# Performance work log

Measured on AMD Instinct MI355X. Metric: run time of the kernel, lower is better.

## Reference

```python
import jax, jax.numpy as jnp
import numpy as np

H = W = 56; WS = 7; SHIFT = 3; NH = 6; DIM = 192; DEPTH = 2
HD = DIM // NH; NW = (H // WS) * (W // WS); N = WS * WS; SCALE = HD ** -0.5

# relative position index (constant, as in WindowAttention.__init__)
_c = np.stack(np.meshgrid(np.arange(WS), np.arange(WS), indexing='ij')).reshape(2, -1)
_r = (_c[:, :, None] - _c[:, None, :]).transpose(1, 2, 0)
_r[..., 0] += WS - 1; _r[..., 1] += WS - 1; _r[..., 0] *= 2 * WS - 1
RPI = jnp.asarray(_r.sum(-1).reshape(-1))  # (N*N,)

def _build_mask():
    # shifted-window attention mask (constant, built in SwinTransformerBlock.__init__)
    img = np.zeros((H, W))
    sl = (slice(0, -WS), slice(-WS, -SHIFT), slice(-SHIFT, None))
    cnt = 0
    for hs in sl:
        for ws_ in sl:
            img[hs, ws_] = cnt; cnt += 1
    mw = img.reshape(H // WS, WS, W // WS, WS).transpose(0, 2, 1, 3).reshape(-1, N)
    am = mw[:, None, :] - mw[:, :, None]  # (nW, N, N)
    return jnp.asarray(np.where(am != 0, -100.0, 0.0).astype(np.float32))

MASK = _build_mask()

def _ln(x, g, b):
    m = jnp.mean(x, -1, keepdims=True)
    v = jnp.mean((x - m) ** 2, -1, keepdims=True)
    return (x - m) * jax.lax.rsqrt(v + 1e-5) * g + b

def setup_inputs() -> dict:
    key = jax.random.key(0)
    ks = jax.random.split(key, 8)
    B = 64; s = 0.02
    return {
        'x': jax.random.normal(ks[0], (B, H * W, DIM), jnp.float32),
        'norm1_g': jnp.ones((DEPTH, DIM), jnp.float32),
        'norm1_b': jnp.zeros((DEPTH, DIM), jnp.float32),
        'qkv_w': jax.random.normal(ks[1], (DEPTH, DIM, 3 * DIM), jnp.float32) * s,
        'qkv_b': jnp.zeros((DEPTH, 3 * DIM), jnp.float32),
        'rpb': jax.random.normal(ks[2], (DEPTH, (2 * WS - 1) ** 2, NH), jnp.float32) * s,
        'proj_w': jax.random.normal(ks[3], (DEPTH, DIM, DIM), jnp.float32) * s,
        'proj_b': jnp.zeros((DEPTH, DIM), jnp.float32),
        'norm2_g': jnp.ones((DEPTH, DIM), jnp.float32),
        'norm2_b': jnp.zeros((DEPTH, DIM), jnp.float32),
        'fc1_w': jax.random.normal(ks[4], (DEPTH, DIM, 4 * DIM), jnp.float32) * s,
        'fc1_b': jnp.zeros((DEPTH, 4 * DIM), jnp.float32),
        'fc2_w': jax.random.normal(ks[5], (DEPTH, 4 * DIM, DIM), jnp.float32) * s,
        'fc2_b': jnp.zeros((DEPTH, DIM), jnp.float32),
    }

def reference(x, norm1_g, norm1_b, qkv_w, qkv_b, rpb, proj_w, proj_b,
              norm2_g, norm2_b, fc1_w, fc1_b, fc2_w, fc2_b):
    B = x.shape[0]
    for i in range(DEPTH):
        shift = 0 if i % 2 == 0 else WS // 2
        # --- windowed MHSA branch ---
        h = _ln(x, norm1_g[i], norm1_b[i]).reshape(B, H, W, DIM)
        if shift:
            h = jnp.roll(h, (-shift, -shift), (1, 2))
        # window partition -> (B*nW, N, C)
        w = h.reshape(B, H // WS, WS, W // WS, WS, DIM)
        w = w.transpose(0, 1, 3, 2, 4, 5).reshape(B * NW, N, DIM)
        qkv = (w @ qkv_w[i] + qkv_b[i]).reshape(B * NW, N, 3, NH, HD)
        qkv = qkv.transpose(2, 0, 3, 1, 4)  # (3, Bw, NH, N, HD)
        q, k, v = qkv[0] * SCALE, qkv[1], qkv[2]
        attn = jnp.einsum('bhnd,bhmd->bhnm', q, k)  # (Bw, NH, N, N)
        bias = rpb[i][RPI].reshape(N, N, NH).transpose(2, 0, 1)
        attn = attn + bias[None]
        if shift:
            attn = attn.reshape(B, NW, NH, N, N) + MASK[None, :, None]
            attn = attn.reshape(B * NW, NH, N, N)
        attn = jax.nn.softmax(attn, axis=-1)
        o = jnp.einsum('bhnm,bhmd->bhnd', attn, v)
        o = o.transpose(0, 2, 1, 3).reshape(B * NW, N, DIM)
        o = o @ proj_w[i] + proj_b[i]
        # window reverse
        h = o.reshape(B, H // WS, W // WS, WS, WS, DIM)
        h = h.transpose(0, 1, 3, 2, 4, 5).reshape(B, H, W, DIM)
        if shift:
            h = jnp.roll(h, (shift, shift), (1, 2))
        x = x + h.reshape(B, H * W, DIM)
        # --- MLP branch ---
        m = _ln(x, norm2_g[i], norm2_b[i])
        m = jax.nn.gelu(m @ fc1_w[i] + fc1_b[i], approximate=False)
        x = x + (m @ fc2_w[i] + fc2_b[i])
    return x
```

## Files before the change

### kernel.cpp

```cpp
#include <hip/hip_runtime.h>
#include <stdint.h>

#define NTOK   49
#define BATCH  64
#define MROWS  (BATCH * 64 * NTOK)
#define SCALE_ 0.17677669529663687f

typedef __attribute__((ext_vector_type(8))) short bf16x8;
typedef __attribute__((ext_vector_type(4))) float f32x4;

union V8 { uint4 u; unsigned short s[8]; };

__device__ __forceinline__ float bf2f(unsigned short u) {
  union { unsigned int i; float f; } c; c.i = ((unsigned int)u) << 16; return c.f;
}
__device__ __forceinline__ unsigned short f2bf(float f) {
  union { float f; unsigned int i; } c; c.f = f;
  unsigned int lsb = (c.i >> 16) & 1;
  return (unsigned short)((c.i + 0x7fffu + lsb) >> 16);
}

__global__ __launch_bounds__(256) void wt_k(const float* __restrict__ W,
    unsigned short* __restrict__ Wt, int K, int N)
{
  int idx = blockIdx.x * 256 + threadIdx.x;
  if (idx < K * N) {
    int k = idx / N, n = idx - k * N;
    Wt[(size_t)n * K + k] = f2bf(W[idx]);
  }
}

__global__ __launch_bounds__(256) void ln_k(const float* __restrict__ X,
    const float* __restrict__ g, const float* __restrict__ b,
    unsigned short* __restrict__ out, int shift)
{
  int wr = blockIdx.x * 4 + (threadIdx.x >> 6);
  int lane = threadIdx.x & 63;
  int win = wr / 49, n = wr % 49;
  int bi = win >> 6, w64 = win & 63;
  int wh = w64 >> 3, ww = w64 & 7;
  int ti = n / 7, tj = n % 7;
  int gh = wh * 7 + ti + shift; if (gh >= 56) gh -= 56;
  int gw = ww * 7 + tj + shift; if (gw >= 56) gw -= 56;
  size_t srow = (size_t)bi * 3136 + gh * 56 + gw;
  const float* xr = X + srow * 192;
  float v0 = xr[lane], v1 = xr[lane + 64], v2 = xr[lane + 128];
  float s  = v0 + v1 + v2;
  float s2 = v0*v0 + v1*v1 + v2*v2;
  #pragma unroll
  for (int m = 32; m >= 1; m >>= 1) { s += __shfl_xor(s, m); s2 += __shfl_xor(s2, m); }
  float mean = s * (1.0f/192.0f);
  float var  = s2 * (1.0f/192.0f) - mean*mean;
  float inv  = rsqrtf(var + 1e-5f);
  unsigned short* orow = out + (size_t)wr * 192;
  orow[lane]       = f2bf((v0-mean)*inv*g[lane]      + b[lane]);
  orow[lane+64]    = f2bf((v1-mean)*inv*g[lane+64]   + b[lane+64]);
  orow[lane+128]   = f2bf((v2-mean)*inv*g[lane+128]  + b[lane+128]);
}

template<int EPI>
__global__ __launch_bounds__(256, 4) void gemm2_k(
    const unsigned short* __restrict__ A,
    const unsigned short* __restrict__ Wt,
    const float* __restrict__ bias,
    unsigned short* __restrict__ Cbf,
    const float* __restrict__ Xres,
    float* __restrict__ Xdst,
    int N, int shift)
{
  __shared__ unsigned short As[128][40];
  const int tid = threadIdx.x;
  const int lane = tid & 63, wv = tid >> 6;
  const int wm = wv >> 1, wn = wv & 1;
  const int row0 = blockIdx.x * 128;
  const int n0   = blockIdx.y * 64;
  const int fr = lane & 15, kq = (lane >> 4) * 8;
  bf16x8 bfr[6][2];
  #pragma unroll
  for (int ks = 0; ks < 6; ++ks)
    #pragma unroll
    for (int ni = 0; ni < 2; ++ni)
      bfr[ks][ni] = *reinterpret_cast<const bf16x8*>(
          &Wt[(size_t)(n0 + wn*32 + ni*16 + fr) * 192 + ks*32 + kq]);
  const int sr  = tid >> 1, ssg = (tid & 1) * 16;
  const unsigned short* arow = A + (size_t)(row0 + sr) * 192 + ssg;
  uint4 a0 = *reinterpret_cast<const uint4*>(arow);
  uint4 a1 = *reinterpret_cast<const uint4*>(arow + 8);
  f32x4 acc[4][2] = {};
  #pragma unroll
  for (int ks = 0; ks < 6; ++ks) {
    __syncthreads();
    *reinterpret_cast<uint4*>(&As[sr][ssg])     = a0;
    *reinterpret_cast<uint4*>(&As[sr][ssg + 8]) = a1;
    if (ks < 5) {
      a0 = *reinterpret_cast<const uint4*>(arow + (ks+1)*32);
      a1 = *reinterpret_cast<const uint4*>(arow + (ks+1)*32 + 8);
    }
    __syncthreads();
    #pragma unroll
    for (int mi = 0; mi < 4; ++mi) {
      bf16x8 afr = *reinterpret_cast<const bf16x8*>(&As[wm*64 + mi*16 + fr][kq]);
      #pragma unroll
      for (int ni = 0; ni < 2; ++ni)
        acc[mi][ni] = __builtin_amdgcn_mfma_f32_16x16x32_bf16(afr, bfr[ks][ni], acc[mi][ni], 0, 0, 0);
    }
  }
  const int lcol = lane & 15, lr4 = (lane >> 4) * 4;
  #pragma unroll
  for (int mi = 0; mi < 4; ++mi)
  #pragma unroll
  for (int ni = 0; ni < 2; ++ni)
  #pragma unroll
  for (int i = 0; i < 4; ++i) {
    int gr = row0 + wm*64 + mi*16 + lr4 + i;
    int gc = n0 + wn*32 + ni*16 + lcol;
    float v = acc[mi][ni][i] + bias[gc];
    if (EPI == 0) {
      Cbf[(size_t)gr * N + gc] = f2bf(v);
    } else {
      int win = gr / 49, n = gr % 49;
      int bi = win >> 6, w64 = win & 63;
      int wh = w64 >> 3, ww = w64 & 7;
      int ti = n / 7, tj = n % 7;
      int gh = wh*7 + ti + shift; if (gh >= 56) gh -= 56;
      int gw = ww*7 + tj + shift; if (gw >= 56) gw -= 56;
      size_t idx = ((size_t)bi * 3136 + gh * 56 + gw) * 192 + gc;
      Xdst[idx] = Xres[idx] + v;
    }
  }
}

__global__ __launch_bounds__(256, 3) void mlp_k(
    const float* __restrict__ X,
    const float* __restrict__ g, const float* __restrict__ b,
    const unsigned short* __restrict__ W1t,
    const float* __restrict__ b1,
    const unsigned short* __restrict__ W2t,
    const float* __restrict__ b2,
    float* __restrict__ Y)
{
  __shared__ unsigned short As[32][200];
  __shared__ unsigned short Hs[32][200];
  const int row0 = blockIdx.x * 32;
  const int tid = threadIdx.x, lane = tid & 63, wv = tid >> 6;
  #pragma unroll
  for (int r = 0; r < 8; ++r) {
    int row = wv * 8 + r;
    const float* xr = X + (size_t)(row0 + row) * 192;
    float v0 = xr[lane], v1 = xr[lane + 64], v2 = xr[lane + 128];
    float s  = v0 + v1 + v2;
    float s2 = v0*v0 + v1*v1 + v2*v2;
    #pragma unroll
    for (int m = 32; m >= 1; m >>= 1) { s += __shfl_xor(s, m); s2 += __shfl_xor(s2, m); }
    float mean = s * (1.0f/192.0f);
    float var  = s2 * (1.0f/192.0f) - mean*mean;
    float inv  = rsqrtf(var + 1e-5f);
    As[row][lane]       = f2bf((v0-mean)*inv*g[lane]      + b[lane]);
    As[row][lane+64]    = f2bf((v1-mean)*inv*g[lane+64]   + b[lane+64]);
    As[row][lane+128]   = f2bf((v2-mean)*inv*g[lane+128]  + b[lane+128]);
  }
  __syncthreads();
  const int fr = lane & 15, kq = (lane >> 4) * 8;
  const int lcol = lane & 15, lr4 = (lane >> 4) * 4;
  f32x4 acc2[2][3] = {};
  #pragma unroll
  for (int q = 0; q < 4; ++q) {
    bf16x8 bw1[6][3];
    #pragma unroll
    for (int ks = 0; ks < 6; ++ks)
      #pragma unroll
      for (int ni = 0; ni < 3; ++ni)
        bw1[ks][ni] = *reinterpret_cast<const bf16x8*>(
            &W1t[(size_t)(q*192 + wv*48 + ni*16 + fr) * 192 + ks*32 + kq]);
    f32x4 acc1[2][3] = {};
    #pragma unroll
    for (int ks = 0; ks < 6; ++ks) {
      #pragma unroll
      for (int mi = 0; mi < 2; ++mi) {
        bf16x8 afr = *reinterpret_cast<const bf16x8*>(&As[mi*16 + fr][ks*32 + kq]);
        #pragma unroll
        for (int ni = 0; ni < 3; ++ni)
          acc1[mi][ni] = __builtin_amdgcn_mfma_f32_16x16x32_bf16(afr, bw1[ks][ni], acc1[mi][ni], 0, 0, 0);
      }
    }
    bf16x8 bw2[6][3];
    #pragma unroll
    for (int ks = 0; ks < 6; ++ks)
      #pragma unroll
      for (int ni = 0; ni < 3; ++ni)
        bw2[ks][ni] = *reinterpret_cast<const bf16x8*>(
            &W2t[(size_t)(wv*48 + ni*16 + fr) * 768 + q*192 + ks*32 + kq]);
    __syncthreads();
    #pragma unroll
    for (int mi = 0; mi < 2; ++mi)
    #pragma unroll
    for (int ni = 0; ni < 3; ++ni)
    #pragma unroll
    for (int i = 0; i < 4; ++i) {
      int rr = mi*16 + lr4 + i;
      int cc = wv*48 + ni*16 + lcol;
      float v = acc1[mi][ni][i] + b1[q*192 + cc];
      float gv = 0.5f * v * (1.0f + erff(v * 0.70710678118654752f));
      Hs[rr][cc] = f2bf(gv);
    }
    __syncthreads();
    #pragma unroll
    for (int ks = 0; ks < 6; ++ks) {
      #pragma unroll
      for (int mi = 0; mi < 2; ++mi) {
        bf16x8 afr = *reinterpret_cast<const bf16x8*>(&Hs[mi*16 + fr][ks*32 + kq]);
        #pragma unroll
        for (int ni = 0; ni < 3; ++ni)
          acc2[mi][ni] = __builtin_amdgcn_mfma_f32_16x16x32_bf16(afr, bw2[ks][ni], acc2[mi][ni], 0, 0, 0);
      }
    }
  }
  #pragma unroll
  for (int mi = 0; mi < 2; ++mi)
  #pragma unroll
  for (int ni = 0; ni < 3; ++ni)
  #pragma unroll
  for (int i = 0; i < 4; ++i) {
    int grow = row0 + mi*16 + lr4 + i;
    int gc = wv*48 + ni*16 + lcol;
    float v = acc2[mi][ni][i] + b2[gc];
    size_t idx = (size_t)grow * 192 + gc;
    Y[idx] = X[idx] + v;
  }
}

template<bool SHIFTED>
__global__ __launch_bounds__(64) void attn_k(
    const unsigned short* __restrict__ qkv,
    const float* __restrict__ rpb,
    unsigned short* __restrict__ out)
{
  __shared__ float kv[2][49][32];
  int blk = blockIdx.x;
  int win = blk / 6, h = blk - win * 6;
  int lane = threadIdx.x;
  const unsigned short* base = qkv + (size_t)win * 49 * 576;
  for (int idx = lane; idx < 196; idx += 64) {
    int n = idx >> 2, sg = (idx & 3) * 8;
    V8 kk, vv;
    kk.u = *reinterpret_cast<const uint4*>(base + n*576 + 192 + h*32 + sg);
    vv.u = *reinterpret_cast<const uint4*>(base + n*576 + 384 + h*32 + sg);
    #pragma unroll
    for (int j = 0; j < 8; ++j) { kv[0][n][sg+j] = bf2f(kk.s[j]); kv[1][n][sg+j] = bf2f(vv.s[j]); }
  }
  __syncthreads();
  if (lane < 49) {
    float q[32];
    const unsigned short* qr = base + (size_t)lane * 576 + h * 32;
    #pragma unroll
    for (int sg = 0; sg < 4; ++sg) {
      V8 qq; qq.u = *reinterpret_cast<const uint4*>(qr + sg*8);
      #pragma unroll
      for (int j = 0; j < 8; ++j) q[sg*8+j] = bf2f(qq.s[j]) * SCALE_;
    }
    int ti = lane / 7, tj = lane - ti * 7;
    int wi = win & 63, wh = wi >> 3, ww = wi & 7;
    int rid = 0;
    if (SHIFTED) {
      int hh = wh*7 + ti, wg = ww*7 + tj;
      rid = (hh < 49 ? 0 : (hh < 53 ? 1 : 2)) * 3 + (wg < 49 ? 0 : (wg < 53 ? 1 : 2));
    }
    float s[49];
    float mx = -1e30f;
    #pragma unroll
    for (int m = 0; m < 49; ++m) {
      float a = 0.f;
      #pragma unroll
      for (int d4 = 0; d4 < 8; ++d4) {
        float4 kf = *reinterpret_cast<const float4*>(&kv[0][m][d4*4]);
        a += q[d4*4+0]*kf.x + q[d4*4+1]*kf.y + q[d4*4+2]*kf.z + q[d4*4+3]*kf.w;
      }
      int mi = m / 7, mj = m - mi * 7;
      a += rpb[((ti - mi + 6) * 13 + (tj - mj + 6)) * 6 + h];
      if (SHIFTED) {
        int hh = wh*7 + mi, wg = ww*7 + mj;
        int rid2 = (hh < 49 ? 0 : (hh < 53 ? 1 : 2)) * 3 + (wg < 49 ? 0 : (wg < 53 ? 1 : 2));
        if (rid2 != rid) a -= 100.f;
      }
      s[m] = a;
      mx = fmaxf(mx, a);
    }
    float sum = 0.f;
    #pragma unroll
    for (int m = 0; m < 49; ++m) { float e = __expf(s[m] - mx); s[m] = e; sum += e; }
    float rs = 1.f / sum;
    float o[32];
    #pragma unroll
    for (int d = 0; d < 32; ++d) o[d] = 0.f;
    #pragma unroll
    for (int m = 0; m < 49; ++m) {
      float p = s[m] * rs;
      #pragma unroll
      for (int d4 = 0; d4 < 8; ++d4) {
        float4 vf = *reinterpret_cast<const float4*>(&kv[1][m][d4*4]);
        o[d4*4+0] += p*vf.x; o[d4*4+1] += p*vf.y; o[d4*4+2] += p*vf.z; o[d4*4+3] += p*vf.w;
      }
    }
    unsigned short* orow = out + ((size_t)win * 49 + lane) * 192 + h * 32;
    #pragma unroll
    for (int sg = 0; sg < 4; ++sg) {
      V8 pk;
      #pragma unroll
      for (int j = 0; j < 8; ++j) pk.s[j] = f2bf(o[sg*8+j]);
      *reinterpret_cast<uint4*>(orow + sg*8) = pk.u;
    }
  }
}

extern "C" void kernel_launch(void* const* d_in, const int* in_sizes, int n_in,
                              void* d_out, int out_size, void* d_ws, size_t ws_size,
                              hipStream_t stream) {
  const float* x    = (const float*)d_in[0];
  const float* n1g  = (const float*)d_in[1];
  const float* n1b  = (const float*)d_in[2];
  const float* qkvw = (const float*)d_in[3];
  const float* qkvb = (const float*)d_in[4];
  const float* rpb  = (const float*)d_in[5];
  const float* pw   = (const float*)d_in[6];
  const float* pb   = (const float*)d_in[7];
  const float* n2g  = (const float*)d_in[8];
  const float* n2b  = (const float*)d_in[9];
  const float* f1w  = (const float*)d_in[10];
  const float* f1b  = (const float*)d_in[11];
  const float* f2w  = (const float*)d_in[12];
  const float* f2b  = (const float*)d_in[13];
  float* out = (float*)d_out;

  const size_t XBYTES = (size_t)MROWS * 192 * 4;
  const size_t ABYTES = (size_t)MROWS * 192 * 2;
  const size_t QBYTES = (size_t)MROWS * 576 * 2;
  char* ws = (char*)d_ws;
  float* x1 = (float*)ws;
  unsigned short* Abuf = (unsigned short*)(ws + XBYTES);
  unsigned short* Bbuf = (unsigned short*)(ws + XBYTES + ABYTES);
  unsigned short* WT   = (unsigned short*)(ws + XBYTES + ABYTES + QBYTES);
  const size_t WQ = 110592, WP = 36864, W1 = 147456, W2 = 147456;
  const size_t WD = WQ + WP + W1 + W2;

  for (int d = 0; d < 2; ++d) {
    unsigned short* wt = WT + d * WD;
    wt_k<<<(int)((WQ + 255)/256), 256, 0, stream>>>(qkvw + (size_t)d*WQ, wt,                 192, 576);
    wt_k<<<(int)((WP + 255)/256), 256, 0, stream>>>(pw   + (size_t)d*WP, wt + WQ,            192, 192);
    wt_k<<<(int)((W1 + 255)/256), 256, 0, stream>>>(f1w  + (size_t)d*W1, wt + WQ + WP,       192, 768);
    wt_k<<<(int)((W2 + 255)/256), 256, 0, stream>>>(f2w  + (size_t)d*W2, wt + WQ + WP + W1,  768, 192);
  }

  const int LNBLK = MROWS / 4;
  const dim3 G_QKV(MROWS/128, 9), G_P(MROWS/128, 3);

  for (int i = 0; i < 2; ++i) {
    int shift = i ? 3 : 0;
    const float* xin = i ? (const float*)x1 : x;
    float* xfin = i ? out : x1;
    const unsigned short* wt = WT + i * WD;
    ln_k<<<LNBLK, 256, 0, stream>>>(xin, n1g + i*192, n1b + i*192, Abuf, shift);
    gemm2_k<0><<<G_QKV, 256, 0, stream>>>(Abuf, wt, qkvb + i*576, Bbuf, nullptr, nullptr, 576, 0);
    if (shift) attn_k<true ><<<BATCH*64*6, 64, 0, stream>>>(Bbuf, rpb + i*169*6, Abuf);
    else       attn_k<false><<<BATCH*64*6, 64, 0, stream>>>(Bbuf, rpb + i*169*6, Abuf);
    gemm2_k<1><<<G_P, 256, 0, stream>>>(Abuf, wt + WQ, pb + i*192, nullptr, xin, x1, 192, shift);
    mlp_k<<<MROWS/32, 256, 0, stream>>>(x1, n2g + i*192, n2b + i*192,
                                        wt + WQ + WP, f1b + i*768,
                                        wt + WQ + WP + W1, f2b + i*192, xfin);
  }
}
```

Baseline: 1.968 ms.

## Fuse LN into QKV GEMM, split MLP into fc1/fc2 with full-K LDS tiles

Layernorm is folded into the QKV and fc1 GEMM kernels, which now hold the whole 128x192 A tile in XOR-swizzled LDS and loop over all output panels in one block. The fused MLP kernel is split into fc1 (writing the GELU hidden tensor to global memory, reusing the QKV buffer) and fc2 (streaming that hidden tensor through LDS with direct global-to-LDS loads). The goal is to drop the separate LN pass and make the MLP's small 32-row tiles more MFMA-efficient. In exchange the hidden activations now make an extra round trip through HBM, and each block keeps a large LDS footprint.

```diff
diff --git a/kernel.cpp b/kernel.cpp
--- a/kernel.cpp
+++ b/kernel.cpp
@@ -1,14 +1,11 @@
 #include <hip/hip_runtime.h>
 #include <stdint.h>
 
-#define NTOK   49
-#define BATCH  64
-#define MROWS  (BATCH * 64 * NTOK)
+#define MROWS  200704
 #define SCALE_ 0.17677669529663687f
 
 typedef __attribute__((ext_vector_type(8))) short bf16x8;
 typedef __attribute__((ext_vector_type(4))) float f32x4;
-
 union V8 { uint4 u; unsigned short s[8]; };
 
 __device__ __forceinline__ float bf2f(unsigned short u) {
@@ -20,6 +17,61 @@
   return (unsigned short)((c.i + 0x7fffu + lsb) >> 16);
 }
 
+typedef __attribute__((address_space(1))) const void gas_t;
+typedef __attribute__((address_space(3))) void las_t;
+__device__ __forceinline__ void gload16(const void* g, void* l) {
+  __builtin_amdgcn_global_load_lds((gas_t*)g, (las_t*)l, 16, 0, 0);
+}
+
+__device__ __forceinline__ bf16x8 ard(const unsigned short* As, int row, int k) {
+  return *reinterpret_cast<const bf16x8*>(As + row * 192 + (((k >> 3) ^ (row & 7)) << 3));
+}
+__device__ __forceinline__ void awr(unsigned short* As, int row, int c, unsigned short v) {
+  As[row * 192 + (((c >> 3) ^ (row & 7)) << 3) + (c & 7)] = v;
+}
+template<int RS>
+__device__ __forceinline__ void stage_a(const unsigned short* __restrict__ src,
+                                        unsigned short* As, int wv, int lane, int colofs) {
+  #pragma unroll
+  for (int i = 0; i < 12; ++i) {
+    int g = wv * 768 + i * 64 + lane;
+    int row = g / 24, c = g - row * 24;
+    int sc = c ^ (row & 7);
+    gload16(src + (size_t)row * RS + colofs + sc * 8, As + (wv * 768 + i * 64) * 8);
+  }
+}
+__device__ __forceinline__ void ln_row(const float* __restrict__ xr,
+    const float* __restrict__ g, const float* __restrict__ b,
+    unsigned short* As, int row, int lane) {
+  float v0 = xr[lane], v1 = xr[lane + 64], v2 = xr[lane + 128];
+  float s  = v0 + v1 + v2;
+  float s2 = v0*v0 + v1*v1 + v2*v2;
+  #pragma unroll
+  for (int m = 32; m >= 1; m >>= 1) { s += __shfl_xor(s, m); s2 += __shfl_xor(s2, m); }
+  float mean = s * (1.0f/192.0f);
+  float var  = s2 * (1.0f/192.0f) - mean*mean;
+  float inv  = rsqrtf(var + 1e-5f);
+  awr(As, row, lane,       f2bf((v0-mean)*inv*g[lane]      + b[lane]));
+  awr(As, row, lane+64,    f2bf((v1-mean)*inv*g[lane+64]   + b[lane+64]));
+  awr(As, row, lane+128,   f2bf((v2-mean)*inv*g[lane+128]  + b[lane+128]));
+}
+__device__ __forceinline__ void panel_mm(const bf16x8 (&afr)[6][4],
+    const unsigned short* __restrict__ Wp, int kq, f32x4 (&acc)[4][2]) {
+  bf16x8 bfr[6][2];
+  #pragma unroll
+  for (int ks = 0; ks < 6; ++ks) {
+    bfr[ks][0] = *reinterpret_cast<const bf16x8*>(Wp + ks*32 + kq);
+    bfr[ks][1] = *reinterpret_cast<const bf16x8*>(Wp + 16*192 + ks*32 + kq);
+  }
+  #pragma unroll
+  for (int ks = 0; ks < 6; ++ks)
+    #pragma unroll
+    for (int mi = 0; mi < 4; ++mi) {
+      acc[mi][0] = __builtin_amdgcn_mfma_f32_16x16x32_bf16(afr[ks][mi], bfr[ks][0], acc[mi][0], 0, 0, 0);
+      acc[mi][1] = __builtin_amdgcn_mfma_f32_16x16x32_bf16(afr[ks][mi], bfr[ks][1], acc[mi][1], 0, 0, 0);
+    }
+}
+
 __global__ __launch_bounds__(256) void wt_k(const float* __restrict__ W,
     unsigned short* __restrict__ Wt, int K, int N)
 {
@@ -30,202 +82,185 @@
   }
 }
 
-__global__ __launch_bounds__(256) void ln_k(const float* __restrict__ X,
+__global__ __launch_bounds__(256, 2) void qkv_k(const float* __restrict__ X,
     const float* __restrict__ g, const float* __restrict__ b,
-    unsigned short* __restrict__ out, int shift)
-{
-  int wr = blockIdx.x * 4 + (threadIdx.x >> 6);
-  int lane = threadIdx.x & 63;
-  int win = wr / 49, n = wr % 49;
-  int bi = win >> 6, w64 = win & 63;
-  int wh = w64 >> 3, ww = w64 & 7;
-  int ti = n / 7, tj = n % 7;
-  int gh = wh * 7 + ti + shift; if (gh >= 56) gh -= 56;
-  int gw = ww * 7 + tj + shift; if (gw >= 56) gw -= 56;
-  size_t srow = (size_t)bi * 3136 + gh * 56 + gw;
-  const float* xr = X + srow * 192;
-  float v0 = xr[lane], v1 = xr[lane + 64], v2 = xr[lane + 128];
-  float s  = v0 + v1 + v2;
-  float s2 = v0*v0 + v1*v1 + v2*v2;
-  #pragma unroll
-  for (int m = 32; m >= 1; m >>= 1) { s += __shfl_xor(s, m); s2 += __shfl_xor(s2, m); }
-  float mean = s * (1.0f/192.0f);
-  float var  = s2 * (1.0f/192.0f) - mean*mean;
-  float inv  = rsqrtf(var + 1e-5f);
-  unsigned short* orow = out + (size_t)wr * 192;
-  orow[lane]       = f2bf((v0-mean)*inv*g[lane]      + b[lane]);
-  orow[lane+64]    = f2bf((v1-mean)*inv*g[lane+64]   + b[lane+64]);
-  orow[lane+128]   = f2bf((v2-mean)*inv*g[lane+128]  + b[lane+128]);
-}
-
-template<int EPI>
-__global__ __launch_bounds__(256, 4) void gemm2_k(
-    const unsigned short* __restrict__ A,
-    const unsigned short* __restrict__ Wt,
-    const float* __restrict__ bias,
-    unsigned short* __restrict__ Cbf,
-    const float* __restrict__ Xres,
-    float* __restrict__ Xdst,
-    int N, int shift)
-{
-  __shared__ unsigned short As[128][40];
-  const int tid = threadIdx.x;
-  const int lane = tid & 63, wv = tid >> 6;
-  const int wm = wv >> 1, wn = wv & 1;
+    const unsigned short* __restrict__ Wt, const float* __restrict__ bias,
+    unsigned short* __restrict__ C, int shift)
+{
+  __shared__ unsigned short As[128 * 192];
+  const int tid = threadIdx.x, lane = tid & 63, wv = tid >> 6;
   const int row0 = blockIdx.x * 128;
-  const int n0   = blockIdx.y * 64;
-  const int fr = lane & 15, kq = (lane >> 4) * 8;
-  bf16x8 bfr[6][2];
+  #pragma unroll 2
+  for (int r = 0; r < 32; ++r) {
+    int row = wv * 32 + r, wr = row0 + row;
+    int win = wr / 49, n = wr - win * 49;
+    int bi = win >> 6, w64 = win & 63, wh = w64 >> 3, ww = w64 & 7;
+    int ti = n / 7, tj = n - ti * 7;
+    int gh = wh*7 + ti + shift; if (gh >= 56) gh -= 56;
+    int gw = ww*7 + tj + shift; if (gw >= 56) gw -= 56;
+    ln_row(X + ((size_t)bi*3136 + gh*56 + gw)*192, g, b, As, row, lane);
+  }
+  __syncthreads();
+  const int wm = wv >> 1, wn = wv & 1, fr = lane & 15, kq = (lane >> 4) * 8;
+  bf16x8 afr[6][4];
   #pragma unroll
   for (int ks = 0; ks < 6; ++ks)
     #pragma unroll
+    for (int mi = 0; mi < 4; ++mi)
+      afr[ks][mi] = ard(As, wm*64 + mi*16 + fr, ks*32 + kq);
+  const int lcol = lane & 15, lr4 = (lane >> 4) * 4;
+  #pragma unroll 2
+  for (int p = 0; p < 9; ++p) {
+    f32x4 acc[4][2] = {};
+    panel_mm(afr, Wt + (size_t)(p*64 + wn*32 + fr) * 192, kq, acc);
+    #pragma unroll
+    for (int mi = 0; mi < 4; ++mi)
+    #pragma unroll
     for (int ni = 0; ni < 2; ++ni)
-      bfr[ks][ni] = *reinterpret_cast<const bf16x8*>(
-          &Wt[(size_t)(n0 + wn*32 + ni*16 + fr) * 192 + ks*32 + kq]);
-  const int sr  = tid >> 1, ssg = (tid & 1) * 16;
-  const unsigned short* arow = A + (size_t)(row0 + sr) * 192 + ssg;
-  uint4 a0 = *reinterpret_cast<const uint4*>(arow);
-  uint4 a1 = *reinterpret_cast<const uint4*>(arow + 8);
-  f32x4 acc[4][2] = {};
-  #pragma unroll
-  for (int ks = 0; ks < 6; ++ks) {
-    __syncthreads();
-    *reinterpret_cast<uint4*>(&As[sr][ssg])     = a0;
-    *reinterpret_cast<uint4*>(&As[sr][ssg + 8]) = a1;
-    if (ks < 5) {
-      a0 = *reinterpret_cast<const uint4*>(arow + (ks+1)*32);
-      a1 = *reinterpret_cast<const uint4*>(arow + (ks+1)*32 + 8);
-    }
-    __syncthreads();
-    #pragma unroll
-    for (int mi = 0; mi < 4; ++mi) {
-      bf16x8 afr = *reinterpret_cast<const bf16x8*>(&As[wm*64 + mi*16 + fr][kq]);
-      #pragma unroll
-      for (int ni = 0; ni < 2; ++ni)
-        acc[mi][ni] = __builtin_amdgcn_mfma_f32_16x16x32_bf16(afr, bfr[ks][ni], acc[mi][ni], 0, 0, 0);
-    }
-  }
+    #pragma unroll
+    for (int i = 0; i < 4; ++i) {
+      int gr = row0 + wm*64 + mi*16 + lr4 + i;
+      int gc = p*64 + wn*32 + ni*16 + lcol;
+      C[(size_t)gr * 576 + gc] = f2bf(acc[mi][ni][i] + bias[gc]);
+    }
+  }
+}
+
+__global__ __launch_bounds__(256, 2) void proj_k(const unsigned short* __restrict__ A,
+    const unsigned short* __restrict__ Wt, const float* __restrict__ bias,
+    const float* __restrict__ Xres, float* __restrict__ Xdst, int shift)
+{
+  __shared__ unsigned short As[128 * 192];
+  const int tid = threadIdx.x, lane = tid & 63, wv = tid >> 6;
+  const int row0 = blockIdx.x * 128;
+  stage_a<192>(A + (size_t)row0 * 192, As, wv, lane, 0);
+  __syncthreads();
+  const int wm = wv >> 1, wn = wv & 1, fr = lane & 15, kq = (lane >> 4) * 8;
+  bf16x8 afr[6][4];
+  #pragma unroll
+  for (int ks = 0; ks < 6; ++ks)
+    #pragma unroll
+    for (int mi = 0; mi < 4; ++mi)
+      afr[ks][mi] = ard(As, wm*64 + mi*16 + fr, ks*32 + kq);
   const int lcol = lane & 15, lr4 = (lane >> 4) * 4;
+  int rbase[16];
   #pragma unroll
   for (int mi = 0; mi < 4; ++mi)
-  #pragma unroll
-  for (int ni = 0; ni < 2; ++ni)
   #pragma unroll
   for (int i = 0; i < 4; ++i) {
     int gr = row0 + wm*64 + mi*16 + lr4 + i;
-    int gc = n0 + wn*32 + ni*16 + lcol;
-    float v = acc[mi][ni][i] + bias[gc];
-    if (EPI == 0) {
-      Cbf[(size_t)gr * N + gc] = f2bf(v);
-    } else {
-      int win = gr / 49, n = gr % 49;
-      int bi = win >> 6, w64 = win & 63;
-      int wh = w64 >> 3, ww = w64 & 7;
-      int ti = n / 7, tj = n % 7;
-      int gh = wh*7 + ti + shift; if (gh >= 56) gh -= 56;
-      int gw = ww*7 + tj + shift; if (gw >= 56) gw -= 56;
-      size_t idx = ((size_t)bi * 3136 + gh * 56 + gw) * 192 + gc;
-      Xdst[idx] = Xres[idx] + v;
-    }
-  }
-}
-
-__global__ __launch_bounds__(256, 3) void mlp_k(
-    const float* __restrict__ X,
+    int win = gr / 49, n = gr - win * 49;
+    int bi = win >> 6, w64 = win & 63, wh = w64 >> 3, ww = w64 & 7;
+    int ti = n / 7, tj = n - ti * 7;
+    int gh = wh*7 + ti + shift; if (gh >= 56) gh -= 56;
+    int gw = ww*7 + tj + shift; if (gw >= 56) gw -= 56;
+    rbase[mi*4 + i] = (bi*3136 + gh*56 + gw) * 192;
+  }
+  #pragma unroll
+  for (int p = 0; p < 3; ++p) {
+    f32x4 acc[4][2] = {};
+    panel_mm(afr, Wt + (size_t)(p*64 + wn*32 + fr) * 192, kq, acc);
+    #pragma unroll
+    for (int mi = 0; mi < 4; ++mi)
+    #pragma unroll
+    for (int ni = 0; ni < 2; ++ni)
+    #pragma unroll
+    for (int i = 0; i < 4; ++i) {
+      int gc = p*64 + wn*32 + ni*16 + lcol;
+      size_t idx = (size_t)rbase[mi*4 + i] + gc;
+      Xdst[idx] = Xres[idx] + acc[mi][ni][i] + bias[gc];
+    }
+  }
+}
+
+__global__ __launch_bounds__(256, 2) void fc1_k(const float* __restrict__ X,
     const float* __restrict__ g, const float* __restrict__ b,
-    const unsigned short* __restrict__ W1t,
-    const float* __restrict__ b1,
-    const unsigned short* __restrict__ W2t,
-    const float* __restrict__ b2,
+    const unsigned short* __restrict__ Wt, const float* __restrict__ bias,
+    unsigned short* __restrict__ H)
+{
+  __shared__ unsigned short As[128 * 192];
+  const int tid = threadIdx.x, lane = tid & 63, wv = tid >> 6;
+  const int row0 = blockIdx.x * 128;
+  #pragma unroll 2
+  for (int r = 0; r < 32; ++r) {
+    int row = wv * 32 + r;
+    ln_row(X + (size_t)(row0 + row) * 192, g, b, As, row, lane);
+  }
+  __syncthreads();
+  const int wm = wv >> 1, wn = wv & 1, fr = lane & 15, kq = (lane >> 4) * 8;
+  bf16x8 afr[6][4];
+  #pragma unroll
+  for (int ks = 0; ks < 6; ++ks)
+    #pragma unroll
+    for (int mi = 0; mi < 4; ++mi)
+      afr[ks][mi] = ard(As, wm*64 + mi*16 + fr, ks*32 + kq);
+  const int lcol = lane & 15, lr4 = (lane >> 4) * 4;
+  #pragma unroll 2
+  for (int p = 0; p < 12; ++p) {
+    f32x4 acc[4][2] = {};
+    panel_mm(afr, Wt + (size_t)(p*64 + wn*32 + fr) * 192, kq, acc);
+    #pragma unroll
+    for (int mi = 0; mi < 4; ++mi)
+    #pragma unroll
+    for (int ni = 0; ni < 2; ++ni)
+    #pragma unroll
+    for (int i = 0; i < 4; ++i) {
+      int gr = row0 + wm*64 + mi*16 + lr4 + i;
+      int gc = p*64 + wn*32 + ni*16 + lcol;
+      float v = acc[mi][ni][i] + bias[gc];
+      float gv = 0.5f * v * (1.0f + erff(v * 0.70710678118654752f));
+      H[(size_t)gr * 768 + gc] = f2bf(gv);
+    }
+  }
+}
+
+__global__ __launch_bounds__(256, 2) void fc2_k(const unsigned short* __restrict__ H,
+    const unsigned short* __restrict__ Wt,
+    const float* __restrict__ bias, const float* __restrict__ Xres,
     float* __restrict__ Y)
 {
-  __shared__ unsigned short As[32][200];
-  __shared__ unsigned short Hs[32][200];
-  const int row0 = blockIdx.x * 32;
+  __shared__ unsigned short As[128 * 192];
   const int tid = threadIdx.x, lane = tid & 63, wv = tid >> 6;
-  #pragma unroll
-  for (int r = 0; r < 8; ++r) {
-    int row = wv * 8 + r;
-    const float* xr = X + (size_t)(row0 + row) * 192;
-    float v0 = xr[lane], v1 = xr[lane + 64], v2 = xr[lane + 128];
-    float s  = v0 + v1 + v2;
-    float s2 = v0*v0 + v1*v1 + v2*v2;
-    #pragma unroll
-    for (int m = 32; m >= 1; m >>= 1) { s += __shfl_xor(s, m); s2 += __shfl_xor(s2, m); }
-    float mean = s * (1.0f/192.0f);
-    float var  = s2 * (1.0f/192.0f) - mean*mean;
-    float inv  = rsqrtf(var + 1e-5f);
-    As[row][lane]       = f2bf((v0-mean)*inv*g[lane]      + b[lane]);
-    As[row][lane+64]    = f2bf((v1-mean)*inv*g[lane+64]   + b[lane+64]);
-    As[row][lane+128]   = f2bf((v2-mean)*inv*g[lane+128]  + b[lane+128]);
-  }
-  __syncthreads();
-  const int fr = lane & 15, kq = (lane >> 4) * 8;
+  const int row0 = blockIdx.x * 128;
+  const int wm = wv >> 1, wn = wv & 1, fr = lane & 15, kq = (lane >> 4) * 8;
+  f32x4 acc[3][4][2] = {};
+  for (int q = 0; q < 4; ++q) {
+    if (q) __syncthreads();
+    stage_a<768>(H + (size_t)row0 * 768, As, wv, lane, q * 192);
+    __syncthreads();
+    #pragma unroll
+    for (int ks = 0; ks < 6; ++ks) {
+      bf16x8 afr[4];
+      #pragma unroll
+      for (int mi = 0; mi < 4; ++mi)
+        afr[mi] = ard(As, wm*64 + mi*16 + fr, ks*32 + kq);
+      #pragma unroll
+      for (int p = 0; p < 3; ++p) {
+        const unsigned short* wp = Wt + (size_t)(p*64 + wn*32 + fr) * 768 + q*192 + ks*32 + kq;
+        bf16x8 b0 = *reinterpret_cast<const bf16x8*>(wp);
+        bf16x8 b1 = *reinterpret_cast<const bf16x8*>(wp + 16*768);
+        #pragma unroll
+        for (int mi = 0; mi < 4; ++mi) {
+          acc[p][mi][0] = __builtin_amdgcn_mfma_f32_16x16x32_bf16(afr[mi], b0, acc[p][mi][0], 0, 0, 0);
+          acc[p][mi][1] = __builtin_amdgcn_mfma_f32_16x16x32_bf16(afr[mi], b1, acc[p][mi][1], 0, 0, 0);
+        }
+      }
+    }
+  }
   const int lcol = lane & 15, lr4 = (lane >> 4) * 4;
-  f32x4 acc2[2][3] = {};
-  #pragma unroll
-  for (int q = 0; q < 4; ++q) {
-    bf16x8 bw1[6][3];
-    #pragma unroll
-    for (int ks = 0; ks < 6; ++ks)
-      #pragma unroll
-      for (int ni = 0; ni < 3; ++ni)
-        bw1[ks][ni] = *reinterpret_cast<const bf16x8*>(
-            &W1t[(size_t)(q*192 + wv*48 + ni*16 + fr) * 192 + ks*32 + kq]);
-    f32x4 acc1[2][3] = {};
-    #pragma unroll
-    for (int ks = 0; ks < 6; ++ks) {
-      #pragma unroll
-      for (int mi = 0; mi < 2; ++mi) {
-        bf16x8 afr = *reinterpret_cast<const bf16x8*>(&As[mi*16 + fr][ks*32 + kq]);
-        #pragma unroll
-        for (int ni = 0; ni < 3; ++ni)
-          acc1[mi][ni] = __builtin_amdgcn_mfma_f32_16x16x32_bf16(afr, bw1[ks][ni], acc1[mi][ni], 0, 0, 0);
-      }
-    }
-    bf16x8 bw2[6][3];
-    #pragma unroll
-    for (int ks = 0; ks < 6; ++ks)
-      #pragma unroll
-      for (int ni = 0; ni < 3; ++ni)
-        bw2[ks][ni] = *reinterpret_cast<const bf16x8*>(
-            &W2t[(size_t)(wv*48 + ni*16 + fr) * 768 + q*192 + ks*32 + kq]);
-    __syncthreads();
-    #pragma unroll
-    for (int mi = 0; mi < 2; ++mi)
-    #pragma unroll
-    for (int ni = 0; ni < 3; ++ni)
-    #pragma unroll
-    for (int i = 0; i < 4; ++i) {
-      int rr = mi*16 + lr4 + i;
-      int cc = wv*48 + ni*16 + lcol;
-      float v = acc1[mi][ni][i] + b1[q*192 + cc];
-      float gv = 0.5f * v * (1.0f + erff(v * 0.70710678118654752f));
-      Hs[rr][cc] = f2bf(gv);
-    }
-    __syncthreads();
-    #pragma unroll
-    for (int ks = 0; ks < 6; ++ks) {
-      #pragma unroll
-      for (int mi = 0; mi < 2; ++mi) {
-        bf16x8 afr = *reinterpret_cast<const bf16x8*>(&Hs[mi*16 + fr][ks*32 + kq]);
-        #pragma unroll
-        for (int ni = 0; ni < 3; ++ni)
-          acc2[mi][ni] = __builtin_amdgcn_mfma_f32_16x16x32_bf16(afr, bw2[ks][ni], acc2[mi][ni], 0, 0, 0);
-      }
-    }
-  }
-  #pragma unroll
-  for (int mi = 0; mi < 2; ++mi)
-  #pragma unroll
-  for (int ni = 0; ni < 3; ++ni)
+  #pragma unroll
+  for (int p = 0; p < 3; ++p)
+  #pragma unroll
+  for (int mi = 0; mi < 4; ++mi)
+  #pragma unroll
+  for (int ni = 0; ni < 2; ++ni)
   #pragma unroll
   for (int i = 0; i < 4; ++i) {
-    int grow = row0 + mi*16 + lr4 + i;
-    int gc = wv*48 + ni*16 + lcol;
-    float v = acc2[mi][ni][i] + b2[gc];
+    int grow = row0 + wm*64 + mi*16 + lr4 + i;
+    int gc = p*64 + wn*32 + ni*16 + lcol;
+    float v = acc[p][mi][ni][i] + bias[gc];
     size_t idx = (size_t)grow * 192 + gc;
-    Y[idx] = X[idx] + v;
+    Y[idx] = Xres[idx] + v;
   }
 }
 
@@ -332,13 +367,14 @@
   float* out = (float*)d_out;
 
   const size_t XBYTES = (size_t)MROWS * 192 * 4;
+  const size_t QBYTES = (size_t)MROWS * 576 * 2;
   const size_t ABYTES = (size_t)MROWS * 192 * 2;
-  const size_t QBYTES = (size_t)MROWS * 576 * 2;
   char* ws = (char*)d_ws;
   float* x1 = (float*)ws;
-  unsigned short* Abuf = (unsigned short*)(ws + XBYTES);
-  unsigned short* Bbuf = (unsigned short*)(ws + XBYTES + ABYTES);
-  unsigned short* WT   = (unsigned short*)(ws + XBYTES + ABYTES + QBYTES);
+  unsigned short* Bbuf = (unsigned short*)(ws + XBYTES);
+  unsigned short* Abuf = (unsigned short*)(ws + XBYTES + QBYTES);
+  unsigned short* Hbuf = Bbuf;
+  unsigned short* WT   = (unsigned short*)(ws + XBYTES + QBYTES + ABYTES);
   const size_t WQ = 110592, WP = 36864, W1 = 147456, W2 = 147456;
   const size_t WD = WQ + WP + W1 + W2;
 
@@ -350,21 +386,18 @@
     wt_k<<<(int)((W2 + 255)/256), 256, 0, stream>>>(f2w  + (size_t)d*W2, wt + WQ + WP + W1,  768, 192);
   }
 
-  const int LNBLK = MROWS / 4;
-  const dim3 G_QKV(MROWS/128, 9), G_P(MROWS/128, 3);
+  const int GB = MROWS / 128;
 
   for (int i = 0; i < 2; ++i) {
     int shift = i ? 3 : 0;
     const float* xin = i ? (const float*)x1 : x;
     float* xfin = i ? out : x1;
     const unsigned short* wt = WT + i * WD;
-    ln_k<<<LNBLK, 256, 0, stream>>>(xin, n1g + i*192, n1b + i*192, Abuf, shift);
-    gemm2_k<0><<<G_QKV, 256, 0, stream>>>(Abuf, wt, qkvb + i*576, Bbuf, nullptr, nullptr, 576, 0);
-    if (shift) attn_k<true ><<<BATCH*64*6, 64, 0, stream>>>(Bbuf, rpb + i*169*6, Abuf);
-    else       attn_k<false><<<BATCH*64*6, 64, 0, stream>>>(Bbuf, rpb + i*169*6, Abuf);
-    gemm2_k<1><<<G_P, 256, 0, stream>>>(Abuf, wt + WQ, pb + i*192, nullptr, xin, x1, 192, shift);
-    mlp_k<<<MROWS/32, 256, 0, stream>>>(x1, n2g + i*192, n2b + i*192,
-                                        wt + WQ + WP, f1b + i*768,
-                                        wt + WQ + WP + W1, f2b + i*192, xfin);
-  }
-}
+    qkv_k<<<GB, 256, 0, stream>>>(xin, n1g + i*192, n1b + i*192, wt, qkvb + i*576, Bbuf, shift);
+    if (shift) attn_k<true ><<<4096*6, 64, 0, stream>>>(Bbuf, rpb + i*169*6, Abuf);
+    else       attn_k<false><<<4096*6, 64, 0, stream>>>(Bbuf, rpb + i*169*6, Abuf);
+    proj_k<<<GB, 256, 0, stream>>>(Abuf, wt + WQ, pb + i*192, xin, x1, shift);
+    fc1_k<<<GB, 256, 0, stream>>>(x1, n2g + i*192, n2b + i*192, wt + WQ + WP, f1b + i*768, Hbuf);
+    fc2_k<<<GB, 256, 0, stream>>>(Hbuf, wt + WQ + WP + W1, f2b + i*192, x1, xfin);
+  }
+}
```

Result: slower. 2.072 ms (+5.3%).
